# Kernel optimization log

Measured on AMD Instinct MI355X. Metric: run time of the kernel, lower is better.

Reference implementation:

```python
import jax, jax.numpy as jnp
import numpy as np

NEG_SLOPE = 0.01  # torch F.leaky_relu default

def _leaky(x):
    return jnp.where(x >= 0, x, NEG_SLOPE * x)

def _gcn(x, W, b, src, dst, w, n):
    # GCNConv(add_self_loops=False, normalize=False):
    # h = x @ W; out[dst] += w * h[src]; out += b
    h = x @ W
    agg = jax.ops.segment_sum(w[:, None] * h[src], dst, num_segments=n)
    return agg + b

def setup_inputs() -> dict:
    key = jax.random.key(0)
    ks = jax.random.split(key, 10)
    N, E, IN, HID, OUT, B = 100000, 300000, 256, 256, 256, 128
    features = jax.random.normal(ks[0], (N, IN), dtype=jnp.float32)
    values = jax.random.uniform(ks[1], (E,), dtype=jnp.float32)
    s = 1.0 / np.sqrt(IN)
    W1 = jax.random.normal(ks[2], (IN, HID), dtype=jnp.float32) * s
    b1 = jnp.zeros((HID,), dtype=jnp.float32)
    W2 = jax.random.normal(ks[3], (HID + IN, OUT), dtype=jnp.float32) * (1.0 / np.sqrt(HID + IN))
    b2 = jnp.zeros((OUT,), dtype=jnp.float32)
    Wl = jax.random.normal(ks[4], (HID + OUT, IN), dtype=jnp.float32) * (1.0 / np.sqrt(HID + OUT))
    bl = jnp.zeros((IN,), dtype=jnp.float32)
    adjs = jax.random.randint(ks[5], (2, E), 0, N, dtype=jnp.int64)
    batch = jnp.sort(jax.random.randint(ks[6], (N,), 0, B, dtype=jnp.int64))
    root_idx = jax.random.randint(ks[7], (B,), 0, N, dtype=jnp.int64)
    return {"features": features, "values": values, "W1": W1, "b1": b1,
            "W2": W2, "b2": b2, "Wl": Wl, "bl": bl,
            "adjs": adjs, "batch": batch, "root_idx": root_idx}

def reference(features, values, W1, b1, W2, b2, Wl, bl, adjs, batch, root_idx):
    N = features.shape[0]
    src, dst = adjs[0], adjs[1]
    f1 = features  # [N, in]
    h = _gcn(f1, W1, b1, src, dst, values, N)  # conv1 -> [N, hid]
    f2 = h
    # root_extend: per-batch broadcast of root features == gather f1[root_idx[batch]]
    root1 = f1[root_idx[batch]]  # [N, in]
    x = _leaky(jnp.concatenate([h, root1], axis=1))
    # dropout is identity at inference
    x = _gcn(x, W2, b2, src, dst, values, N)  # conv2 -> [N, out]
    x = _leaky(x)
    root2 = f2[root_idx[batch]]  # [N, hid]
    x = jnp.concatenate([x, root2], axis=1)
    return _leaky(x @ Wl + bl)  # [N, in]
```

## Files before the change

kernel.cpp:

```cpp
#include <hip/hip_runtime.h>

typedef short short8 __attribute__((ext_vector_type(8)));
typedef float floatx4 __attribute__((ext_vector_type(4)));

#define LEAKY(v) ((v) >= 0.0f ? (v) : 0.01f * (v))

constexpr int D = 256;

__device__ __forceinline__ short f2bf(float x) {
  unsigned u = __float_as_uint(x);
  u += 0x7fffu + ((u >> 16) & 1u);
  return (short)(u >> 16);
}
__device__ __forceinline__ float bf2f(short s) {
  return __uint_as_float(((unsigned)(unsigned short)s) << 16);
}

#define AS1 __attribute__((address_space(1)))
#define AS3 __attribute__((address_space(3)))

__device__ __forceinline__ void gload_lds16(const void* g, void* lds) {
  __builtin_amdgcn_global_load_lds((const AS1 void*)g, (AS3 void*)lds, 16, 0, 0);
}

__global__ void transpose_w(const float* __restrict__ W1,
                            const float* __restrict__ W2,
                            const float* __restrict__ Wl,
                            short* __restrict__ Wt) {
  __shared__ float t[32][33];
  const float* src = (blockIdx.z == 0) ? W1 : (blockIdx.z == 1) ? W2 : Wl;
  short* dst = Wt + (size_t)blockIdx.z * D * D;
  int tx = threadIdx.x, ty = threadIdx.y;
  t[ty][tx] = src[(size_t)(blockIdx.y * 32 + ty) * D + blockIdx.x * 32 + tx];
  __syncthreads();
  dst[(size_t)(blockIdx.x * 32 + ty) * D + blockIdx.y * 32 + tx] =
      f2bf(t[tx][ty]);
}

template <bool A_F32, bool ADD_ROW, bool FINAL>
__global__ __launch_bounds__(512, 4) void gemm_tile(
    const void* __restrict__ Avoid, const short* __restrict__ Wt,
    const float* __restrict__ R, const int* __restrict__ batch,
    const float* __restrict__ bias, void* __restrict__ Cvoid, int M) {
  __shared__ __align__(16) short As[64 * 256];
  const int tid = threadIdx.x;
  const int l = tid & 63, w = tid >> 6, lm = l & 15, q = l >> 4;
  const int ncol0 = w * 32;
  const int rowBase = blockIdx.x * 64;

  short8 bf[2][8];
#pragma unroll
  for (int j = 0; j < 2; j++)
#pragma unroll
    for (int kk = 0; kk < 8; kk++)
      bf[j][kk] = *(const short8*)(Wt + (size_t)(ncol0 + j * 16 + lm) * D +
                                   kk * 32 + q * 8);

#pragma unroll
  for (int r = 0; r < 4; r++) {
    const int s = r * 8 + w;
    const int kk = s >> 2, i = s & 3;
    int grow = rowBase + i * 16 + lm;
    grow = grow < M ? grow : M - 1;
    if (A_F32) {
      const float* ap = (const float*)Avoid + (size_t)grow * D + kk * 32 + q * 8;
      float4 v0 = ((const float4*)ap)[0];
      float4 v1 = ((const float4*)ap)[1];
      short8 sv;
      sv[0] = f2bf(v0.x); sv[1] = f2bf(v0.y); sv[2] = f2bf(v0.z); sv[3] = f2bf(v0.w);
      sv[4] = f2bf(v1.x); sv[5] = f2bf(v1.y); sv[6] = f2bf(v1.z); sv[7] = f2bf(v1.w);
      *(short8*)((char*)As + s * 1024 + l * 16) = sv;
    } else {
      const char* src =
          (const char*)Avoid + (size_t)grow * 512 + kk * 64 + q * 16;
      gload_lds16(src, (char*)As + s * 1024);
    }
  }
  __syncthreads();

  floatx4 acc[4][2];
#pragma unroll
  for (int i = 0; i < 4; i++)
#pragma unroll
    for (int j = 0; j < 2; j++) acc[i][j] = (floatx4){0.f, 0.f, 0.f, 0.f};

  const char* base = (const char*)As + (size_t)l * 16;
#pragma unroll
  for (int kk = 0; kk < 8; kk++) {
    short8 a[4];
#pragma unroll
    for (int i = 0; i < 4; i++)
      a[i] = *(const short8*)(base + (kk * 4 + i) * 1024);
#pragma unroll
    for (int i = 0; i < 4; i++)
#pragma unroll
      for (int j = 0; j < 2; j++)
        acc[i][j] = __builtin_amdgcn_mfma_f32_16x16x32_bf16(
            bf[j][kk], a[i], acc[i][j], 0, 0, 0);
  }

  float4 b4[2];
  if (FINAL) {
#pragma unroll
    for (int j = 0; j < 2; j++)
      b4[j] = *(const float4*)(bias + ncol0 + j * 16 + q * 4);
  }
#pragma unroll
  for (int i = 0; i < 4; i++) {
    const int row = rowBase + i * 16 + lm;
    if (row < M) {
      int rb = 0;
      if (ADD_ROW) rb = batch[row];
#pragma unroll
      for (int j = 0; j < 2; j++) {
        const int col0 = ncol0 + j * 16 + q * 4;
        float c0 = acc[i][j][0], c1 = acc[i][j][1], c2 = acc[i][j][2],
              c3 = acc[i][j][3];
        if (ADD_ROW) {
          float4 rv = *(const float4*)(R + (size_t)rb * D + col0);
          c0 += rv.x; c1 += rv.y; c2 += rv.z; c3 += rv.w;
        }
        if (!FINAL) {
          uint2 o;
          o.x = (unsigned)(unsigned short)f2bf(c0) |
                ((unsigned)(unsigned short)f2bf(c1) << 16);
          o.y = (unsigned)(unsigned short)f2bf(c2) |
                ((unsigned)(unsigned short)f2bf(c3) << 16);
          *(uint2*)((short*)Cvoid + (size_t)row * D + col0) = o;
        } else {
          c0 += b4[j].x; c1 += b4[j].y; c2 += b4[j].z; c3 += b4[j].w;
          c0 = LEAKY(c0); c1 = LEAKY(c1); c2 = LEAKY(c2); c3 = LEAKY(c3);
          float4 o = {c0, c1, c2, c3};
          *(float4*)((float*)Cvoid + (size_t)row * D + col0) = o;
        }
      }
    }
  }
}

__global__ void count_dst(const int* __restrict__ dst, int* __restrict__ offs,
                          int E) {
  int e = blockIdx.x * 256 + threadIdx.x;
  if (e < E) atomicAdd(&offs[dst[e]], 1);
}

__global__ void scan_blocks(int* __restrict__ offs, int* __restrict__ bsums,
                            int n) {
  __shared__ int tmp[256];
  int i = blockIdx.x * 256 + threadIdx.x;
  int v = (i < n) ? offs[i] : 0;
  tmp[threadIdx.x] = v;
  __syncthreads();
  for (int off = 1; off < 256; off <<= 1) {
    int t = (threadIdx.x >= off) ? tmp[threadIdx.x - off] : 0;
    __syncthreads();
    tmp[threadIdx.x] += t;
    __syncthreads();
  }
  if (i < n) offs[i] = tmp[threadIdx.x] - v;
  if (threadIdx.x == 255) bsums[blockIdx.x] = tmp[255];
}

__global__ void scan_sums(int* __restrict__ bs, int nb) {
  __shared__ int tmp[1024];
  int v = (threadIdx.x < nb) ? bs[threadIdx.x] : 0;
  tmp[threadIdx.x] = v;
  __syncthreads();
  for (int off = 1; off < 1024; off <<= 1) {
    int t = (threadIdx.x >= off) ? tmp[threadIdx.x - off] : 0;
    __syncthreads();
    tmp[threadIdx.x] += t;
    __syncthreads();
  }
  if (threadIdx.x < nb) bs[threadIdx.x] = tmp[threadIdx.x] - v;
}

__global__ void add_offsets(int* __restrict__ offs, const int* __restrict__ bs,
                            int n, int* __restrict__ cursor) {
  int i = blockIdx.x * 256 + threadIdx.x;
  if (i < n) {
    int o = offs[i] + bs[blockIdx.x];
    offs[i] = o;
    cursor[i] = o;
  }
}

__global__ void fill_buckets(const int* __restrict__ src,
                             const int* __restrict__ dst,
                             const float* __restrict__ vals,
                             int* __restrict__ cursor, int* __restrict__ esrc,
                             float* __restrict__ ew, int E) {
  int e = blockIdx.x * 256 + threadIdx.x;
  if (e < E) {
    int p = atomicAdd(&cursor[dst[e]], 1);
    esrc[p] = src[e];
    ew[p] = vals[e];
  }
}

__global__ __launch_bounds__(256) void aggregate_bf(
    const short* __restrict__ H, const int* __restrict__ offs,
    const int* __restrict__ esrc, const float* __restrict__ ew,
    const float* __restrict__ bias, short* __restrict__ out, int N, int E) {
  int node = blockIdx.x * 4 + (threadIdx.x >> 6);
  if (node >= N) return;
  int lane = threadIdx.x & 63;
  int beg = offs[node];
  int end = (node == N - 1) ? E : offs[node + 1];
  float a0 = 0.f, a1 = 0.f, a2 = 0.f, a3 = 0.f;
  for (int i = beg; i < end; i++) {
    int s = esrc[i];
    float wv = ew[i];
    uint2 pk = ((const uint2*)(H + (size_t)s * D))[lane];
    a0 += wv * bf2f((short)(pk.x & 0xffff));
    a1 += wv * bf2f((short)(pk.x >> 16));
    a2 += wv * bf2f((short)(pk.y & 0xffff));
    a3 += wv * bf2f((short)(pk.y >> 16));
  }
  float4 b = ((const float4*)bias)[lane];
  a0 = LEAKY(a0 + b.x);
  a1 = LEAKY(a1 + b.y);
  a2 = LEAKY(a2 + b.z);
  a3 = LEAKY(a3 + b.w);
  uint2 o;
  o.x = (unsigned)(unsigned short)f2bf(a0) |
        ((unsigned)(unsigned short)f2bf(a1) << 16);
  o.y = (unsigned)(unsigned short)f2bf(a2) |
        ((unsigned)(unsigned short)f2bf(a3) << 16);
  ((uint2*)(out + (size_t)node * D))[lane] = o;
}

__global__ void root_gemm1(const float* __restrict__ X,
                           const int* __restrict__ root_idx,
                           const float* __restrict__ W2,
                           float* __restrict__ R1) {
  __shared__ float a[D];
  int b = blockIdx.x, j = threadIdx.x;
  int r = root_idx[b];
  a[j] = LEAKY(X[(size_t)r * D + j]);
  __syncthreads();
  float acc = 0.f;
#pragma unroll 8
  for (int k = 0; k < D; k++) acc += a[k] * W2[(size_t)(D + k) * D + j];
  R1[b * D + j] = acc;
}

__global__ void root_gemm2(const short* __restrict__ H,
                           const int* __restrict__ root_idx,
                           const int* __restrict__ offs,
                           const int* __restrict__ esrc,
                           const float* __restrict__ ew,
                           const float* __restrict__ b1,
                           const float* __restrict__ Wl, float* __restrict__ R2,
                           int N, int E) {
  __shared__ float a[D];
  int b = blockIdx.x, j = threadIdx.x;
  int r = root_idx[b];
  int beg = offs[r], end = (r == N - 1) ? E : offs[r + 1];
  float acc = b1[j];
  for (int e = beg; e < end; e++)
    acc += ew[e] * bf2f(H[(size_t)esrc[e] * D + j]);
  a[j] = acc;
  __syncthreads();
  float s = 0.f;
#pragma unroll 8
  for (int k = 0; k < D; k++) s += a[k] * Wl[(size_t)(D + k) * D + j];
  R2[b * D + j] = s;
}

extern "C" void kernel_launch(void* const* d_in, const int* in_sizes, int n_in,
                              void* d_out, int out_size, void* d_ws,
                              size_t ws_size, hipStream_t stream) {
  const float* features = (const float*)d_in[0];
  const float* values   = (const float*)d_in[1];
  const float* W1 = (const float*)d_in[2];
  const float* b1 = (const float*)d_in[3];
  const float* W2 = (const float*)d_in[4];
  const float* b2 = (const float*)d_in[5];
  const float* Wl = (const float*)d_in[6];
  const float* bl = (const float*)d_in[7];
  const int* adjs = (const int*)d_in[8];
  const int* batch = (const int*)d_in[9];
  const int* root_idx = (const int*)d_in[10];

  const int N = in_sizes[0] / D;
  const int E = in_sizes[1];
  const int B = in_sizes[10];
  const int* srcI = adjs;
  const int* dstI = adjs + E;

  short* bf0 = (short*)d_ws;
  short* bf1 = bf0 + (size_t)N * D;
  short* Wt = bf1 + (size_t)N * D;
  float* R1 = (float*)(Wt + (size_t)3 * D * D);
  float* R2 = R1 + (size_t)B * D;
  float* ew = R2 + (size_t)B * D;
  int* offs = (int*)(ew + E);
  int* cursor = offs + N;
  int* esrc = cursor + N;
  int* bsums = esrc + E;

  const int nb = (N + 255) / 256;

  hipMemsetAsync(offs, 0, (size_t)N * sizeof(int), stream);
  count_dst<<<(E + 255) / 256, 256, 0, stream>>>(dstI, offs, E);
  scan_blocks<<<nb, 256, 0, stream>>>(offs, bsums, N);
  scan_sums<<<1, 1024, 0, stream>>>(bsums, nb);
  add_offsets<<<nb, 256, 0, stream>>>(offs, bsums, N, cursor);
  fill_buckets<<<(E + 255) / 256, 256, 0, stream>>>(srcI, dstI, values, cursor,
                                                    esrc, ew, E);

  transpose_w<<<dim3(8, 8, 3), dim3(32, 32), 0, stream>>>(W1, W2, Wl, Wt);

  const int ggrid = (N + 63) / 64;
  const int aggGrid = (N + 3) / 4;

  gemm_tile<true, false, false><<<ggrid, 512, 0, stream>>>(
      features, Wt, nullptr, nullptr, nullptr, bf0, N);

  aggregate_bf<<<aggGrid, 256, 0, stream>>>(bf0, offs, esrc, ew, b1, bf1, N, E);

  root_gemm1<<<B, 256, 0, stream>>>(features, root_idx, W2, R1);
  root_gemm2<<<B, 256, 0, stream>>>(bf0, root_idx, offs, esrc, ew, b1, Wl, R2,
                                    N, E);

  gemm_tile<false, true, false><<<ggrid, 512, 0, stream>>>(
      bf1, Wt + (size_t)D * D, R1, batch, nullptr, bf0, N);

  aggregate_bf<<<aggGrid, 256, 0, stream>>>(bf0, offs, esrc, ew, b2, bf1, N, E);

  gemm_tile<false, true, true><<<ggrid, 512, 0, stream>>>(
      bf1, Wt + (size_t)2 * D * D, R2, batch, bl, (float*)d_out, N);
}
```

Baseline: 493.5 us.

## Replace LDS-staged GEMM tiles with register-direct 16-row strip loop

Replaces the 64-row tile GEMM, which staged A through shared memory with a barrier, with a grid-stride loop over 16-row strips. Each wave loads its A fragments straight from global memory into registers and runs the MFMAs without shared memory or synchronisation. The per-wave weight fragments stay in registers across strips, and launch bounds are relaxed to 2 blocks per CU. In exchange, all eight waves in a block read the same A rows, so it relies on cache hits for that duplicated traffic, and occupancy may drop.

```diff
diff --git a/kernel.cpp b/kernel.cpp
--- a/kernel.cpp
+++ b/kernel.cpp
@@ -14,13 +14,6 @@
 }
 __device__ __forceinline__ float bf2f(short s) {
   return __uint_as_float(((unsigned)(unsigned short)s) << 16);
-}
-
-#define AS1 __attribute__((address_space(1)))
-#define AS3 __attribute__((address_space(3)))
-
-__device__ __forceinline__ void gload_lds16(const void* g, void* lds) {
-  __builtin_amdgcn_global_load_lds((const AS1 void*)g, (AS3 void*)lds, 16, 0, 0);
 }
 
 __global__ void transpose_w(const float* __restrict__ W1,
@@ -38,66 +31,24 @@
 }
 
 template <bool A_F32, bool ADD_ROW, bool FINAL>
-__global__ __launch_bounds__(512, 4) void gemm_tile(
+__global__ __launch_bounds__(512, 2) void gemm_strip(
     const void* __restrict__ Avoid, const short* __restrict__ Wt,
     const float* __restrict__ R, const int* __restrict__ batch,
-    const float* __restrict__ bias, void* __restrict__ Cvoid, int M) {
-  __shared__ __align__(16) short As[64 * 256];
+    const float* __restrict__ bias, void* __restrict__ Cvoid, int M,
+    int nStrips) {
   const int tid = threadIdx.x;
   const int l = tid & 63, w = tid >> 6, lm = l & 15, q = l >> 4;
   const int ncol0 = w * 32;
-  const int rowBase = blockIdx.x * 64;
 
   short8 bf[2][8];
 #pragma unroll
   for (int j = 0; j < 2; j++)
 #pragma unroll
-    for (int kk = 0; kk < 8; kk++)
+    for (int kk = 0; kk < 8; kk++) {
       bf[j][kk] = *(const short8*)(Wt + (size_t)(ncol0 + j * 16 + lm) * D +
                                    kk * 32 + q * 8);
-
-#pragma unroll
-  for (int r = 0; r < 4; r++) {
-    const int s = r * 8 + w;
-    const int kk = s >> 2, i = s & 3;
-    int grow = rowBase + i * 16 + lm;
-    grow = grow < M ? grow : M - 1;
-    if (A_F32) {
-      const float* ap = (const float*)Avoid + (size_t)grow * D + kk * 32 + q * 8;
-      float4 v0 = ((const float4*)ap)[0];
-      float4 v1 = ((const float4*)ap)[1];
-      short8 sv;
-      sv[0] = f2bf(v0.x); sv[1] = f2bf(v0.y); sv[2] = f2bf(v0.z); sv[3] = f2bf(v0.w);
-      sv[4] = f2bf(v1.x); sv[5] = f2bf(v1.y); sv[6] = f2bf(v1.z); sv[7] = f2bf(v1.w);
-      *(short8*)((char*)As + s * 1024 + l * 16) = sv;
-    } else {
-      const char* src =
-          (const char*)Avoid + (size_t)grow * 512 + kk * 64 + q * 16;
-      gload_lds16(src, (char*)As + s * 1024);
+      asm volatile("" : "+v"(bf[j][kk]));
     }
-  }
-  __syncthreads();
-
-  floatx4 acc[4][2];
-#pragma unroll
-  for (int i = 0; i < 4; i++)
-#pragma unroll
-    for (int j = 0; j < 2; j++) acc[i][j] = (floatx4){0.f, 0.f, 0.f, 0.f};
-
-  const char* base = (const char*)As + (size_t)l * 16;
-#pragma unroll
-  for (int kk = 0; kk < 8; kk++) {
-    short8 a[4];
-#pragma unroll
-    for (int i = 0; i < 4; i++)
-      a[i] = *(const short8*)(base + (kk * 4 + i) * 1024);
-#pragma unroll
-    for (int i = 0; i < 4; i++)
-#pragma unroll
-      for (int j = 0; j < 2; j++)
-        acc[i][j] = __builtin_amdgcn_mfma_f32_16x16x32_bf16(
-            bf[j][kk], a[i], acc[i][j], 0, 0, 0);
-  }
 
   float4 b4[2];
   if (FINAL) {
@@ -105,17 +56,50 @@
     for (int j = 0; j < 2; j++)
       b4[j] = *(const float4*)(bias + ncol0 + j * 16 + q * 4);
   }
-#pragma unroll
-  for (int i = 0; i < 4; i++) {
-    const int row = rowBase + i * 16 + lm;
+
+  for (int sp = blockIdx.x; sp < nStrips; sp += gridDim.x) {
+    const int row = sp * 16 + lm;
+    const int rl = row < M ? row : M - 1;
+
+    short8 a[8];
+    if (A_F32) {
+      const float* ap = (const float*)Avoid + (size_t)rl * D + q * 8;
+#pragma unroll
+      for (int kk = 0; kk < 8; kk++) {
+        float4 v0 = *(const float4*)(ap + (size_t)kk * 32);
+        float4 v1 = *(const float4*)(ap + (size_t)kk * 32 + 4);
+        short8 sv;
+        sv[0] = f2bf(v0.x); sv[1] = f2bf(v0.y); sv[2] = f2bf(v0.z); sv[3] = f2bf(v0.w);
+        sv[4] = f2bf(v1.x); sv[5] = f2bf(v1.y); sv[6] = f2bf(v1.z); sv[7] = f2bf(v1.w);
+        a[kk] = sv;
+        asm volatile("" : "+v"(a[kk]));
+      }
+    } else {
+      const short* ap = (const short*)Avoid + (size_t)rl * D + q * 8;
+#pragma unroll
+      for (int kk = 0; kk < 8; kk++) {
+        a[kk] = *(const short8*)(ap + (size_t)kk * 32);
+        asm volatile("" : "+v"(a[kk]));
+      }
+    }
+
+    floatx4 acc[2];
+    acc[0] = (floatx4){0.f, 0.f, 0.f, 0.f};
+    acc[1] = (floatx4){0.f, 0.f, 0.f, 0.f};
+#pragma unroll
+    for (int kk = 0; kk < 8; kk++)
+#pragma unroll
+      for (int j = 0; j < 2; j++)
+        acc[j] = __builtin_amdgcn_mfma_f32_16x16x32_bf16(bf[j][kk], a[kk],
+                                                         acc[j], 0, 0, 0);
+
     if (row < M) {
       int rb = 0;
       if (ADD_ROW) rb = batch[row];
 #pragma unroll
       for (int j = 0; j < 2; j++) {
         const int col0 = ncol0 + j * 16 + q * 4;
-        float c0 = acc[i][j][0], c1 = acc[i][j][1], c2 = acc[i][j][2],
-              c3 = acc[i][j][3];
+        float c0 = acc[j][0], c1 = acc[j][1], c2 = acc[j][2], c3 = acc[j][3];
         if (ADD_ROW) {
           float4 rv = *(const float4*)(R + (size_t)rb * D + col0);
           c0 += rv.x; c1 += rv.y; c2 += rv.z; c3 += rv.w;
@@ -312,11 +296,12 @@
 
   transpose_w<<<dim3(8, 8, 3), dim3(32, 32), 0, stream>>>(W1, W2, Wl, Wt);
 
-  const int ggrid = (N + 63) / 64;
+  const int nStrips = (N + 15) / 16;
+  const int sgrid = (nStrips + 3) / 4;
   const int aggGrid = (N + 3) / 4;
 
-  gemm_tile<true, false, false><<<ggrid, 512, 0, stream>>>(
-      features, Wt, nullptr, nullptr, nullptr, bf0, N);
+  gemm_strip<true, false, false><<<sgrid, 512, 0, stream>>>(
+      features, Wt, nullptr, nullptr, nullptr, bf0, N, nStrips);
 
   aggregate_bf<<<aggGrid, 256, 0, stream>>>(bf0, offs, esrc, ew, b1, bf1, N, E);
 
@@ -324,11 +309,11 @@
   root_gemm2<<<B, 256, 0, stream>>>(bf0, root_idx, offs, esrc, ew, b1, Wl, R2,
                                     N, E);
 
-  gemm_tile<false, true, false><<<ggrid, 512, 0, stream>>>(
-      bf1, Wt + (size_t)D * D, R1, batch, nullptr, bf0, N);
+  gemm_strip<false, true, false><<<sgrid, 512, 0, stream>>>(
+      bf1, Wt + (size_t)D * D, R1, batch, nullptr, bf0, N, nStrips);
 
   aggregate_bf<<<aggGrid, 256, 0, stream>>>(bf0, offs, esrc, ew, b2, bf1, N, E);
 
-  gemm_tile<false, true, true><<<ggrid, 512, 0, stream>>>(
-      bf1, Wt + (size_t)2 * D * D, R2, batch, bl, (float*)d_out, N);
-}
+  gemm_strip<false, true, true><<<sgrid, 512, 0, stream>>>(
+      bf1, Wt + (size_t)2 * D * D, R2, batch, bl, (float*)d_out, N, nStrips);
+}
```

Result: slower. 641.3 us (+30.0%).

## Make GEMMs persistent with double-buffered LDS prefetch and pre-convert features to bf16

Applied to the files above, without the earlier changes.

Replaces the one-tile-per-block GEMM with a persistent kernel on a fixed grid of 256 blocks. Each block loads its weight fragments into registers once, then loops over row tiles, double-buffering the A tile in LDS so the next tile's global-to-LDS load overlaps the current tile's MFMA work. This removes the per-tile weight reload and exposes load latency hiding. The first layer's fp32 features now go through a separate conversion kernel into bf16, which costs an extra read and write pass of the feature matrix. There is also a risk of a race: only one __syncthreads per iteration guards the swap between the staging buffer and the compute buffer.

```diff
diff --git a/kernel.cpp b/kernel.cpp
--- a/kernel.cpp
+++ b/kernel.cpp
@@ -37,16 +37,31 @@
       f2bf(t[tx][ty]);
 }
 
-template <bool A_F32, bool ADD_ROW, bool FINAL>
-__global__ __launch_bounds__(512, 4) void gemm_tile(
-    const void* __restrict__ Avoid, const short* __restrict__ Wt,
+__global__ __launch_bounds__(256) void conv_bf(const float* __restrict__ X,
+                                               short* __restrict__ Y,
+                                               long n8) {
+  long i = (long)blockIdx.x * 256 + threadIdx.x;
+  const long stride = (long)gridDim.x * 256;
+  for (; i < n8; i += stride) {
+    float4 v0 = ((const float4*)X)[2 * i];
+    float4 v1 = ((const float4*)X)[2 * i + 1];
+    short8 s;
+    s[0] = f2bf(v0.x); s[1] = f2bf(v0.y); s[2] = f2bf(v0.z); s[3] = f2bf(v0.w);
+    s[4] = f2bf(v1.x); s[5] = f2bf(v1.y); s[6] = f2bf(v1.z); s[7] = f2bf(v1.w);
+    ((short8*)Y)[i] = s;
+  }
+}
+
+template <bool ADD_ROW, bool FINAL>
+__global__ __launch_bounds__(512, 2) void gemm_pipe(
+    const short* __restrict__ A, const short* __restrict__ Wt,
     const float* __restrict__ R, const int* __restrict__ batch,
-    const float* __restrict__ bias, void* __restrict__ Cvoid, int M) {
-  __shared__ __align__(16) short As[64 * 256];
+    const float* __restrict__ bias, void* __restrict__ Cvoid, int M,
+    int nTiles) {
+  __shared__ __align__(16) short As[2][64 * 256];
   const int tid = threadIdx.x;
   const int l = tid & 63, w = tid >> 6, lm = l & 15, q = l >> 4;
   const int ncol0 = w * 32;
-  const int rowBase = blockIdx.x * 64;
 
   short8 bf[2][8];
 #pragma unroll
@@ -55,49 +70,11 @@
     for (int kk = 0; kk < 8; kk++)
       bf[j][kk] = *(const short8*)(Wt + (size_t)(ncol0 + j * 16 + lm) * D +
                                    kk * 32 + q * 8);
-
-#pragma unroll
-  for (int r = 0; r < 4; r++) {
-    const int s = r * 8 + w;
-    const int kk = s >> 2, i = s & 3;
-    int grow = rowBase + i * 16 + lm;
-    grow = grow < M ? grow : M - 1;
-    if (A_F32) {
-      const float* ap = (const float*)Avoid + (size_t)grow * D + kk * 32 + q * 8;
-      float4 v0 = ((const float4*)ap)[0];
-      float4 v1 = ((const float4*)ap)[1];
-      short8 sv;
-      sv[0] = f2bf(v0.x); sv[1] = f2bf(v0.y); sv[2] = f2bf(v0.z); sv[3] = f2bf(v0.w);
-      sv[4] = f2bf(v1.x); sv[5] = f2bf(v1.y); sv[6] = f2bf(v1.z); sv[7] = f2bf(v1.w);
-      *(short8*)((char*)As + s * 1024 + l * 16) = sv;
-    } else {
-      const char* src =
-          (const char*)Avoid + (size_t)grow * 512 + kk * 64 + q * 16;
-      gload_lds16(src, (char*)As + s * 1024);
-    }
-  }
-  __syncthreads();
-
-  floatx4 acc[4][2];
-#pragma unroll
-  for (int i = 0; i < 4; i++)
-#pragma unroll
-    for (int j = 0; j < 2; j++) acc[i][j] = (floatx4){0.f, 0.f, 0.f, 0.f};
-
-  const char* base = (const char*)As + (size_t)l * 16;
-#pragma unroll
-  for (int kk = 0; kk < 8; kk++) {
-    short8 a[4];
-#pragma unroll
-    for (int i = 0; i < 4; i++)
-      a[i] = *(const short8*)(base + (kk * 4 + i) * 1024);
-#pragma unroll
-    for (int i = 0; i < 4; i++)
-#pragma unroll
-      for (int j = 0; j < 2; j++)
-        acc[i][j] = __builtin_amdgcn_mfma_f32_16x16x32_bf16(
-            bf[j][kk], a[i], acc[i][j], 0, 0, 0);
-  }
+#pragma unroll
+  for (int j = 0; j < 2; j++)
+#pragma unroll
+    for (int kk = 0; kk < 8; kk++)
+      asm volatile("" : "+v"(bf[j][kk]));
 
   float4 b4[2];
   if (FINAL) {
@@ -105,36 +82,84 @@
     for (int j = 0; j < 2; j++)
       b4[j] = *(const float4*)(bias + ncol0 + j * 16 + q * 4);
   }
-#pragma unroll
-  for (int i = 0; i < 4; i++) {
-    const int row = rowBase + i * 16 + lm;
-    if (row < M) {
-      int rb = 0;
-      if (ADD_ROW) rb = batch[row];
-#pragma unroll
-      for (int j = 0; j < 2; j++) {
-        const int col0 = ncol0 + j * 16 + q * 4;
-        float c0 = acc[i][j][0], c1 = acc[i][j][1], c2 = acc[i][j][2],
-              c3 = acc[i][j][3];
-        if (ADD_ROW) {
-          float4 rv = *(const float4*)(R + (size_t)rb * D + col0);
-          c0 += rv.x; c1 += rv.y; c2 += rv.z; c3 += rv.w;
-        }
-        if (!FINAL) {
-          uint2 o;
-          o.x = (unsigned)(unsigned short)f2bf(c0) |
-                ((unsigned)(unsigned short)f2bf(c1) << 16);
-          o.y = (unsigned)(unsigned short)f2bf(c2) |
-                ((unsigned)(unsigned short)f2bf(c3) << 16);
-          *(uint2*)((short*)Cvoid + (size_t)row * D + col0) = o;
-        } else {
-          c0 += b4[j].x; c1 += b4[j].y; c2 += b4[j].z; c3 += b4[j].w;
-          c0 = LEAKY(c0); c1 = LEAKY(c1); c2 = LEAKY(c2); c3 = LEAKY(c3);
-          float4 o = {c0, c1, c2, c3};
-          *(float4*)((float*)Cvoid + (size_t)row * D + col0) = o;
+
+  const int stride = gridDim.x;
+  int t = blockIdx.x;
+  int p = 0;
+
+  auto stage = [&](int tile, int buf) {
+#pragma unroll
+    for (int r = 0; r < 4; r++) {
+      const int s = r * 8 + w;
+      const int kk = s >> 2, i = s & 3;
+      int grow = tile * 64 + i * 16 + lm;
+      grow = grow < M ? grow : M - 1;
+      const char* src = (const char*)A + (size_t)grow * 512 + kk * 64 + q * 16;
+      gload_lds16(src, (char*)(&As[buf][0]) + s * 1024);
+    }
+  };
+
+  if (t < nTiles) stage(t, 0);
+
+  for (; t < nTiles; t += stride) {
+    __syncthreads();
+    const int nxt = t + stride;
+    if (nxt < nTiles) stage(nxt, p ^ 1);
+
+    floatx4 acc[4][2];
+#pragma unroll
+    for (int i = 0; i < 4; i++)
+#pragma unroll
+      for (int j = 0; j < 2; j++) acc[i][j] = (floatx4){0.f, 0.f, 0.f, 0.f};
+
+    const char* base = (const char*)(&As[p][0]) + (size_t)l * 16;
+#pragma unroll
+    for (int kk = 0; kk < 8; kk++) {
+      short8 a[4];
+#pragma unroll
+      for (int i = 0; i < 4; i++)
+        a[i] = *(const short8*)(base + (kk * 4 + i) * 1024);
+#pragma unroll
+      for (int i = 0; i < 4; i++)
+#pragma unroll
+        for (int j = 0; j < 2; j++)
+          acc[i][j] = __builtin_amdgcn_mfma_f32_16x16x32_bf16(
+              bf[j][kk], a[i], acc[i][j], 0, 0, 0);
+    }
+
+    const int rowBase = t * 64;
+#pragma unroll
+    for (int i = 0; i < 4; i++) {
+      const int row = rowBase + i * 16 + lm;
+      if (row < M) {
+        int rb = 0;
+        if (ADD_ROW) rb = batch[row];
+#pragma unroll
+        for (int j = 0; j < 2; j++) {
+          const int col0 = ncol0 + j * 16 + q * 4;
+          float c0 = acc[i][j][0], c1 = acc[i][j][1], c2 = acc[i][j][2],
+                c3 = acc[i][j][3];
+          if (ADD_ROW) {
+            float4 rv = *(const float4*)(R + (size_t)rb * D + col0);
+            c0 += rv.x; c1 += rv.y; c2 += rv.z; c3 += rv.w;
+          }
+          if (!FINAL) {
+            uint2 o;
+            o.x = (unsigned)(unsigned short)f2bf(c0) |
+                  ((unsigned)(unsigned short)f2bf(c1) << 16);
+            o.y = (unsigned)(unsigned short)f2bf(c2) |
+                  ((unsigned)(unsigned short)f2bf(c3) << 16);
+            *(uint2*)((short*)Cvoid + (size_t)row * D + col0) = o;
+          } else {
+            c0 += b4[j].x; c1 += b4[j].y; c2 += b4[j].z; c3 += b4[j].w;
+            c0 = LEAKY(c0); c1 = LEAKY(c1); c2 = LEAKY(c2); c3 = LEAKY(c3);
+            float4 o = {c0, c1, c2, c3};
+            *(float4*)((float*)Cvoid + (size_t)row * D + col0) = o;
+          }
         }
       }
     }
+    p ^= 1;
   }
 }
 
@@ -312,11 +337,14 @@
 
   transpose_w<<<dim3(8, 8, 3), dim3(32, 32), 0, stream>>>(W1, W2, Wl, Wt);
 
-  const int ggrid = (N + 63) / 64;
+  conv_bf<<<2048, 256, 0, stream>>>(features, bf1, (long)N * D / 8);
+
+  const int nTiles = (N + 63) / 64;
+  const int ggrid = 256;
   const int aggGrid = (N + 3) / 4;
 
-  gemm_tile<true, false, false><<<ggrid, 512, 0, stream>>>(
-      features, Wt, nullptr, nullptr, nullptr, bf0, N);
+  gemm_pipe<false, false><<<ggrid, 512, 0, stream>>>(
+      bf1, Wt, nullptr, nullptr, nullptr, bf0, N, nTiles);
 
   aggregate_bf<<<aggGrid, 256, 0, stream>>>(bf0, offs, esrc, ew, b1, bf1, N, E);
 
@@ -324,11 +352,11 @@
   root_gemm2<<<B, 256, 0, stream>>>(bf0, root_idx, offs, esrc, ew, b1, Wl, R2,
                                     N, E);
 
-  gemm_tile<false, true, false><<<ggrid, 512, 0, stream>>>(
-      bf1, Wt + (size_t)D * D, R1, batch, nullptr, bf0, N);
+  gemm_pipe<true, false><<<ggrid, 512, 0, stream>>>(
+      bf1, Wt + (size_t)D * D, R1, batch, nullptr, bf0, N, nTiles);
 
   aggregate_bf<<<aggGrid, 256, 0, stream>>>(bf0, offs, esrc, ew, b2, bf1, N, E);
 
-  gemm_tile<false, true, true><<<ggrid, 512, 0, stream>>>(
-      bf1, Wt + (size_t)2 * D * D, R2, batch, bl, (float*)d_out, N);
-}
+  gemm_pipe<true, true><<<ggrid, 512, 0, stream>>>(
+      bf1, Wt + (size_t)2 * D * D, R2, batch, bl, (float*)d_out, N, nTiles);
+}
```

After: 479.8 us. 2.8% less time.
